# Optimization experiments

Hardware: AMD Instinct MI355X
Metric: run time of the kernel (lower is better)

## Reference

```python
import jax, jax.numpy as jnp
import numpy as np

TOP_K = 6
ROUTED_SCALE = 2.5

def setup_inputs() -> dict:
    key = jax.random.key(0)
    ks = jax.random.split(key, 8)
    T, H, I, E = 1024, 2048, 1024, 16
    Is = 2 * I  # shared expert intermediate = n_shared_experts * moe_intermediate_size
    s = 0.02
    return {
        "hidden_states": jax.random.normal(ks[0], (T, H), jnp.float32),
        "gate_w": jax.random.normal(ks[1], (E, H), jnp.float32) * s,          # ReplicatedLinear [out,in]
        "e_score_correction_bias": jax.random.normal(ks[2], (E,), jnp.float32) * s,
        "w1": jax.random.normal(ks[3], (E, 2 * I, H), jnp.float32) * s,       # merged gate_up per expert
        "w2": jax.random.normal(ks[4], (E, H, I), jnp.float32) * s,           # down proj per expert
        "shared_w1": jax.random.normal(ks[5], (2 * Is, H), jnp.float32) * s,  # shared gate_up
        "shared_w2": jax.random.normal(ks[6], (H, Is), jnp.float32) * s,      # shared down
    }

def _silu_and_mul(gu):
    g, u = jnp.split(gu, 2, axis=-1)
    return jax.nn.silu(g) * u

def _moe_forward(hidden_states, gate_w, e_score_correction_bias, w1, w2, shared_w1, shared_w2):
    T, H = hidden_states.shape
    E = gate_w.shape[0]
    # shared expert path (Dots1MLP)
    shared_out = _silu_and_mul(hidden_states @ shared_w1.T) @ shared_w2.T  # [T,H]
    # gating in fp32 (moe_gating_fp32=True)
    router_logits = hidden_states.astype(jnp.float32) @ gate_w.astype(jnp.float32).T  # [T,E]
    # noaux_tc routing: sigmoid scores + correction bias for selection, raw sigmoid for weights
    scores = jax.nn.sigmoid(router_logits)
    choice = scores + e_score_correction_bias[None, :]
    _, topk_idx = jax.lax.top_k(choice, TOP_K)                              # [T,k]
    topk_w = jnp.take_along_axis(scores, topk_idx, axis=1)                  # [T,k]
    topk_w = topk_w / jnp.sum(topk_w, axis=-1, keepdims=True)
    topk_w = topk_w * ROUTED_SCALE
    # dense combine weights [T,E] (top-k slots per token, rest zero)
    route_w = jnp.zeros((T, E), jnp.float32)
    route_w = route_w.at[jnp.arange(T)[:, None], topk_idx].set(topk_w)
    # expert MLPs (computed for all experts, masked by routing weights)
    gu = jnp.einsum('th,egh->teg', hidden_states, w1)                       # [T,E,2I]
    h = _silu_and_mul(gu)                                                   # [T,E,I]
    routed_out = jnp.einsum('tei,ehi,te->th', h, w2, route_w.astype(hidden_states.dtype))
    return routed_out + shared_out                                          # [T,H]

def reference(hidden_states, gate_w, e_score_correction_bias, w1, w2, shared_w1, shared_w2):
    return _moe_forward(hidden_states, gate_w, e_score_correction_bias, w1, w2, shared_w1, shared_w2)
```

## Files before the change

kernel.cpp:

```cpp
#include <hip/hip_runtime.h>
#include <hip/hip_bf16.h>

#define T_TOK 1024
#define NEXP 16
#define HD 2048
#define TOPK 6

typedef __attribute__((ext_vector_type(8))) short short8;
typedef __attribute__((ext_vector_type(4))) float floatx4;

__device__ __forceinline__ short f2bf(float f) {
    unsigned u = __builtin_bit_cast(unsigned, f);
    u += 0x7FFFu + ((u >> 16) & 1u);
    return (short)(u >> 16);
}

typedef __attribute__((address_space(1))) void gvoid;
typedef __attribute__((address_space(3))) void lvoid;
__device__ __forceinline__ void gload_lds16(const void* g, void* l) {
    __builtin_amdgcn_global_load_lds((gvoid*)g, (lvoid*)l, 16, 0, 0);
}

#define WAITCNT_VM4 0x0F74
#define WAITCNT_VM0 0x0F70

__global__ __launch_bounds__(256) void router_cvt(
    const float* __restrict__ X, const float* __restrict__ GW,
    const float* __restrict__ bias, int* __restrict__ counts,
    int* __restrict__ lists, int* __restrict__ tok_e,
    int* __restrict__ tok_pos, float* __restrict__ tok_w,
    const float* __restrict__ W1, const float* __restrict__ W2,
    const float* __restrict__ SW1, const float* __restrict__ SW2,
    short* __restrict__ Xb, short* __restrict__ W1b, short* __restrict__ W2b,
    short* __restrict__ SW1b, short* __restrict__ SW2b)
{
    if (blockIdx.x < 256) {
        const int wave = threadIdx.x >> 6;
        const int l = threadIdx.x & 63;
        const int t = blockIdx.x * 4 + wave;
        const float* x = X + (size_t)t * HD;
        float acc[NEXP];
#pragma unroll
        for (int e = 0; e < NEXP; ++e) acc[e] = 0.f;
        for (int k = l; k < HD; k += 64) {
            const float xv = x[k];
#pragma unroll
            for (int e = 0; e < NEXP; ++e) acc[e] += xv * GW[e * HD + k];
        }
#pragma unroll
        for (int e = 0; e < NEXP; ++e) {
            float v = acc[e];
#pragma unroll
            for (int m = 32; m >= 1; m >>= 1) v += __shfl_xor(v, m, 64);
            acc[e] = v;
        }
        if (l == 0) {
            float s[NEXP], choice[NEXP];
#pragma unroll
            for (int e = 0; e < NEXP; ++e) {
                s[e] = 1.f / (1.f + __expf(-acc[e]));
                choice[e] = s[e] + bias[e];
            }
            int idx[TOPK]; float wv[TOPK]; float wsum = 0.f;
            bool used[NEXP];
#pragma unroll
            for (int e = 0; e < NEXP; ++e) used[e] = false;
            for (int j = 0; j < TOPK; ++j) {
                float best = -1e30f; int bi = 0;
                for (int e = 0; e < NEXP; ++e)
                    if (!used[e] && choice[e] > best) { best = choice[e]; bi = e; }
                used[bi] = true; idx[j] = bi; wv[j] = s[bi]; wsum += s[bi];
            }
            const float scale = 2.5f / wsum;
            for (int j = 0; j < TOPK; ++j) {
                const int e = idx[j];
                const int pos = atomicAdd(&counts[e], 1);
                lists[e * T_TOK + pos] = t;
                tok_e[t * TOPK + j] = e;
                tok_pos[t * TOPK + j] = pos;
                tok_w[t * TOPK + j] = wv[j] * scale;
            }
        }
        return;
    }
    const int C0 = 262144;
    const int C1 = C0 + 8388608;
    const int C2 = C1 + 4194304;
    const int C3 = C2 + 1048576;
    const int C4 = C3 + 524288;
    const int stride = (gridDim.x - 256) * 256;
#pragma unroll 2
    for (int i = (int)(blockIdx.x - 256) * 256 + (int)threadIdx.x; i < C4;
         i += stride) {
        const float* s; short* d; int l;
        if (i < C0)      { s = X;   d = Xb;   l = i; }
        else if (i < C1) { s = W1;  d = W1b;  l = i - C0; }
        else if (i < C2) { s = W2;  d = W2b;  l = i - C1; }
        else if (i < C3) { s = SW1; d = SW1b; l = i - C2; }
        else             { s = SW2; d = SW2b; l = i - C3; }
        const floatx4 v0 = __builtin_nontemporal_load(((const floatx4*)s) + 2 * l);
        const floatx4 v1 = __builtin_nontemporal_load(((const floatx4*)s) + 2 * l + 1);
        short8 o;
        o[0] = f2bf(v0[0]); o[1] = f2bf(v0[1]); o[2] = f2bf(v0[2]); o[3] = f2bf(v0[3]);
        o[4] = f2bf(v1[0]); o[5] = f2bf(v1[1]); o[6] = f2bf(v1[2]); o[7] = f2bf(v1[3]);
        ((short8*)d)[l] = o;
    }
}

__global__ __launch_bounds__(256) void offsets_descs(
    const int* __restrict__ counts, int* __restrict__ offs,
    int* __restrict__ gu, int* __restrict__ gu_n,
    int* __restrict__ dn, int* __restrict__ dn_n)
{
    __shared__ int base_gu[NEXP], base_dn[NEXP], nys[NEXP];
    if (threadIdx.x == 0) {
        int a = 0, bg = 256, bd = 128;
        for (int e = 0; e < NEXP; ++e) {
            offs[e] = a; a += counts[e];
            const int ny = (counts[e] + 127) >> 7;
            nys[e] = ny; base_gu[e] = bg; base_dn[e] = bd;
            bg += ny * 16; bd += ny * 16;
        }
        *gu_n = bg; *dn_n = bd;
    }
    __syncthreads();
    for (int i = threadIdx.x; i < 256; i += 256)
        gu[i] = (NEXP << 16) | ((i >> 5) << 8) | (i & 31);
    for (int i = threadIdx.x; i < 128; i += 256)
        dn[i] = (NEXP << 16) | ((i >> 4) << 8) | (i & 15);
    for (int e = 0; e < NEXP; ++e) {
        const int nt = nys[e] * 16;
        for (int i = threadIdx.x; i < nt; i += 256) {
            const int v = (e << 16) | ((i >> 4) << 8) | (i & 15);
            gu[base_gu[e] + i] = v;
            dn[base_dn[e] + i] = v;
        }
    }
}

__global__ __launch_bounds__(256) void gateup3(
    const short* __restrict__ Xbf, const short* __restrict__ W1bf,
    const short* __restrict__ SW1bf,
    const int* __restrict__ counts, const int* __restrict__ offs,
    const int* __restrict__ lists, const int* __restrict__ descs,
    const int* __restrict__ ndesc,
    short* __restrict__ h_r, short* __restrict__ h_s)
{
    __shared__ short sA[3][128][32];
    __shared__ short sB[3][128][32];
    if ((int)blockIdx.x >= *ndesc) return;
    const int d = descs[blockIdx.x];
    const int z = d >> 16, yb = (d >> 8) & 255, xb = d & 255;
    const bool shx = (z == NEXP);
    const int cnt = shx ? T_TOK : counts[z];
    const int m0 = yb * 128;
    if (m0 >= cnt) return;
    const int Ih = shx ? 2048 : 1024;
    const int i0 = xb * 64;
    const short* W = shx ? SW1bf : (W1bf + (size_t)z * 2048 * HD);
    short* Hout = shx ? h_s : h_r;
    const int hbase = shx ? 0 : offs[z];

    const int tid = threadIdx.x;
    const int wave = tid >> 6, lane = tid & 63;
    const int srow0 = wave * 32 + (lane >> 2);
    const int srow1 = srow0 + 16;
    const int scol = ((lane & 3) ^ ((lane >> 3) & 3)) * 8;

    int ar0 = m0 + srow0; if (ar0 > cnt - 1) ar0 = cnt - 1;
    int ar1 = m0 + srow1; if (ar1 > cnt - 1) ar1 = cnt - 1;
    const int tok0 = shx ? ar0 : lists[z * T_TOK + ar0];
    const int tok1 = shx ? ar1 : lists[z * T_TOK + ar1];
    const short* ag0 = Xbf + (size_t)tok0 * HD + scol;
    const short* ag1 = Xbf + (size_t)tok1 * HD + scol;
    const int br0 = (srow0 < 64) ? (i0 + srow0) : (Ih + i0 + srow0 - 64);
    const int br1 = (srow1 < 64) ? (i0 + srow1) : (Ih + i0 + srow1 - 64);
    const short* bg0 = W + (size_t)br0 * HD + scol;
    const short* bg1 = W + (size_t)br1 * HD + scol;

    const int wx = wave & 1, wy = wave >> 1;
    const int l15 = lane & 15, l4 = lane >> 4;
    const int fcol = (l4 ^ ((l15 >> 1) & 3)) * 8;

    floatx4 acc[4][4];
#pragma unroll
    for (int a = 0; a < 4; ++a)
#pragma unroll
        for (int b = 0; b < 4; ++b) acc[a][b] = (floatx4){0.f, 0.f, 0.f, 0.f};

    const int nsteps = HD / 32;
#pragma unroll
    for (int pb = 0; pb < 2; ++pb) {
        const int off = pb * 32;
        gload_lds16(ag0 + off, &sA[pb][wave * 32][0]);
        gload_lds16(ag1 + off, &sA[pb][wave * 32 + 16][0]);
        gload_lds16(bg0 + off, &sB[pb][wave * 32][0]);
        gload_lds16(bg1 + off, &sB[pb][wave * 32 + 16][0]);
    }

    int p = 0, q = 2;
    for (int s = 0; s < nsteps; ++s) {
        if (s + 1 < nsteps) __builtin_amdgcn_s_waitcnt(WAITCNT_VM4);
        else                __builtin_amdgcn_s_waitcnt(WAITCNT_VM0);
        __builtin_amdgcn_s_barrier();
        if (s + 2 < nsteps) {
            const int off = (s + 2) * 32;
            gload_lds16(ag0 + off, &sA[q][wave * 32][0]);
            gload_lds16(ag1 + off, &sA[q][wave * 32 + 16][0]);
            gload_lds16(bg0 + off, &sB[q][wave * 32][0]);
            gload_lds16(bg1 + off, &sB[q][wave * 32 + 16][0]);
        }
        short8 af[4], bfr[4];
#pragma unroll
        for (int mc = 0; mc < 4; ++mc)
            af[mc] = *(const short8*)&sA[p][wy * 64 + mc * 16 + l15][fcol];
#pragma unroll
        for (int cb = 0; cb < 4; ++cb) {
            const int br = ((cb < 2) ? 0 : 64) + wx * 32 + (cb & 1) * 16 + l15;
            bfr[cb] = *(const short8*)&sB[p][br][fcol];
        }
#pragma unroll
        for (int mc = 0; mc < 4; ++mc)
#pragma unroll
            for (int cb = 0; cb < 4; ++cb)
                acc[mc][cb] = __builtin_amdgcn_mfma_f32_16x16x32_bf16(
                    af[mc], bfr[cb], acc[mc][cb], 0, 0, 0);
        p = (p == 2) ? 0 : p + 1;
        q = (q == 2) ? 0 : q + 1;
    }

#pragma unroll
    for (int mc = 0; mc < 4; ++mc)
#pragma unroll
        for (int cb = 0; cb < 2; ++cb)
#pragma unroll
            for (int r = 0; r < 4; ++r) {
                const int mrel = wy * 64 + mc * 16 + l4 * 4 + r;
                if (m0 + mrel < cnt) {
                    const float g = acc[mc][cb][r];
                    const float u = acc[mc][cb + 2][r];
                    const float h = g / (1.f + __expf(-g)) * u;
                    const int col = i0 + wx * 32 + cb * 16 + l15;
                    Hout[(size_t)(hbase + m0 + mrel) * Ih + col] = f2bf(h);
                }
            }
}

__global__ __launch_bounds__(256) void down3(
    const short* __restrict__ h_r, const short* __restrict__ h_s,
    const short* __restrict__ W2bf, const short* __restrict__ SW2bf,
    const int* __restrict__ counts, const int* __restrict__ offs,
    const int* __restrict__ descs, const int* __restrict__ ndesc,
    float* __restrict__ h2, float* __restrict__ sh_out)
{
    __shared__ short sA[3][128][32];
    __shared__ short sB[3][128][32];
    if ((int)blockIdx.x >= *ndesc) return;
    const int d = descs[blockIdx.x];
    const int z = d >> 16, yb = (d >> 8) & 255, xb = d & 255;
    const bool shx = (z == NEXP);
    const int cnt = shx ? T_TOK : counts[z];
    const int m0 = yb * 128;
    if (m0 >= cnt) return;
    const int Kih = shx ? 2048 : 1024;
    const int n0 = xb * 128;
    const short* A = shx ? h_s : h_r;
    const short* W = shx ? SW2bf : (W2bf + (size_t)z * HD * 1024);
    float* outb = shx ? sh_out : h2;
    const int hbase = shx ? 0 : offs[z];

    const int tid = threadIdx.x;
    const int wave = tid >> 6, lane = tid & 63;
    const int srow0 = wave * 32 + (lane >> 2);
    const int srow1 = srow0 + 16;
    const int scol = ((lane & 3) ^ ((lane >> 3) & 3)) * 8;

    int ar0 = m0 + srow0; if (ar0 > cnt - 1) ar0 = cnt - 1;
    int ar1 = m0 + srow1; if (ar1 > cnt - 1) ar1 = cnt - 1;
    const short* ag0 = A + (size_t)(hbase + ar0) * Kih + scol;
    const short* ag1 = A + (size_t)(hbase + ar1) * Kih + scol;
    const short* bg0 = W + (size_t)(n0 + srow0) * Kih + scol;
    const short* bg1 = W + (size_t)(n0 + srow1) * Kih + scol;

    const int wx = wave & 1, wy = wave >> 1;
    const int l15 = lane & 15, l4 = lane >> 4;
    const int fcol = (l4 ^ ((l15 >> 1) & 3)) * 8;

    floatx4 acc[4][4];
#pragma unroll
    for (int a = 0; a < 4; ++a)
#pragma unroll
        for (int b = 0; b < 4; ++b) acc[a][b] = (floatx4){0.f, 0.f, 0.f, 0.f};

    const int nsteps = Kih / 32;
#pragma unroll
    for (int pb = 0; pb < 2; ++pb) {
        const int off = pb * 32;
        gload_lds16(ag0 + off, &sA[pb][wave * 32][0]);
        gload_lds16(ag1 + off, &sA[pb][wave * 32 + 16][0]);
        gload_lds16(bg0 + off, &sB[pb][wave * 32][0]);
        gload_lds16(bg1 + off, &sB[pb][wave * 32 + 16][0]);
    }

    int p = 0, q = 2;
    for (int s = 0; s < nsteps; ++s) {
        if (s + 1 < nsteps) __builtin_amdgcn_s_waitcnt(WAITCNT_VM4);
        else                __builtin_amdgcn_s_waitcnt(WAITCNT_VM0);
        __builtin_amdgcn_s_barrier();
        if (s + 2 < nsteps) {
            const int off = (s + 2) * 32;
            gload_lds16(ag0 + off, &sA[q][wave * 32][0]);
            gload_lds16(ag1 + off, &sA[q][wave * 32 + 16][0]);
            gload_lds16(bg0 + off, &sB[q][wave * 32][0]);
            gload_lds16(bg1 + off, &sB[q][wave * 32 + 16][0]);
        }
        short8 af[4], bfr[4];
#pragma unroll
        for (int mc = 0; mc < 4; ++mc)
            af[mc] = *(const short8*)&sA[p][wy * 64 + mc * 16 + l15][fcol];
#pragma unroll
        for (int cb = 0; cb < 4; ++cb)
            bfr[cb] = *(const short8*)&sB[p][wx * 64 + cb * 16 + l15][fcol];
#pragma unroll
        for (int mc = 0; mc < 4; ++mc)
#pragma unroll
            for (int cb = 0; cb < 4; ++cb)
                acc[mc][cb] = __builtin_amdgcn_mfma_f32_16x16x32_bf16(
                    af[mc], bfr[cb], acc[mc][cb], 0, 0, 0);
        p = (p == 2) ? 0 : p + 1;
        q = (q == 2) ? 0 : q + 1;
    }

#pragma unroll
    for (int mc = 0; mc < 4; ++mc)
#pragma unroll
        for (int r = 0; r < 4; ++r) {
            const int mrel = wy * 64 + mc * 16 + l4 * 4 + r;
            if (m0 + mrel >= cnt) continue;
            float* orow = outb + (size_t)(hbase + m0 + mrel) * HD + n0 + wx * 64 + l15;
#pragma unroll
            for (int cb = 0; cb < 4; ++cb)
                orow[cb * 16] = acc[mc][cb][r];
        }
}

__global__ __launch_bounds__(256) void combine_kernel(
    const float* __restrict__ h2, const float* __restrict__ sh_out,
    const int* __restrict__ offs, const int* __restrict__ tok_e,
    const int* __restrict__ tok_pos, const float* __restrict__ tok_w,
    float* __restrict__ out)
{
    const int t = blockIdx.x;
    int rows[TOPK]; float w[TOPK];
#pragma unroll
    for (int j = 0; j < TOPK; ++j) {
        const int e = tok_e[t * TOPK + j];
        rows[j] = offs[e] + tok_pos[t * TOPK + j];
        w[j] = tok_w[t * TOPK + j];
    }
    for (int c = threadIdx.x * 4; c < HD; c += 256 * 4) {
        float4 acc = *(const float4*)(sh_out + (size_t)t * HD + c);
#pragma unroll
        for (int j = 0; j < TOPK; ++j) {
            const float4 v = *(const float4*)(h2 + (size_t)rows[j] * HD + c);
            acc.x += w[j] * v.x; acc.y += w[j] * v.y;
            acc.z += w[j] * v.z; acc.w += w[j] * v.w;
        }
        *(float4*)(out + (size_t)t * HD + c) = acc;
    }
}

extern "C" void kernel_launch(void* const* d_in, const int* in_sizes, int n_in,
                              void* d_out, int out_size, void* d_ws, size_t ws_size,
                              hipStream_t stream) {
    const float* X    = (const float*)d_in[0];
    const float* GW   = (const float*)d_in[1];
    const float* BIAS = (const float*)d_in[2];
    const float* W1   = (const float*)d_in[3];
    const float* W2   = (const float*)d_in[4];
    const float* SW1  = (const float*)d_in[5];
    const float* SW2  = (const float*)d_in[6];
    float* out = (float*)d_out;

    char* ws = (char*)d_ws;
    int*   counts  = (int*)(ws + 0);
    int*   offs    = (int*)(ws + 64);
    int*   lists   = (int*)(ws + 256);
    int*   tok_e   = (int*)(ws + 65792);
    int*   tok_pos = (int*)(ws + 90368);
    float* tok_w   = (float*)(ws + 114944);
    int*   gu_n    = (int*)(ws + 139776);
    int*   dn_n    = (int*)(ws + 139780);
    int*   gu_desc = (int*)(ws + 139840);
    int*   dn_desc = (int*)(ws + 145024);
    short* h_r     = (short*)(ws + 262144);
    short* h_s     = (short*)(ws + 12845056);
    float* h2      = (float*)(ws + 17039360);
    float* sh_out  = (float*)(ws + 67371008);
    short* Xbf     = (short*)(ws + 75759616);
    short* W1bf    = (short*)(ws + 79953920);
    short* W2bf    = (short*)(ws + 214171648);
    short* SW1bf   = (short*)(ws + 281280512);
    short* SW2bf   = (short*)(ws + 298057728);
    const size_t WS_NEEDED = 306446336;
    if (ws_size < WS_NEEDED) return;

    hipMemsetAsync(counts, 0, 64, stream);
    router_cvt<<<4352, 256, 0, stream>>>(X, GW, BIAS, counts, lists,
                                         tok_e, tok_pos, tok_w,
                                         W1, W2, SW1, SW2,
                                         Xbf, W1bf, W2bf, SW1bf, SW2bf);
    offsets_descs<<<1, 256, 0, stream>>>(counts, offs, gu_desc, gu_n,
                                         dn_desc, dn_n);

    gateup3<<<1280, 256, 0, stream>>>(Xbf, W1bf, SW1bf, counts, offs, lists,
                                      gu_desc, gu_n, h_r, h_s);
    down3<<<1152, 256, 0, stream>>>(h_r, h_s, W2bf, SW2bf, counts, offs,
                                    dn_desc, dn_n, h2, sh_out);
    combine_kernel<<<T_TOK, 256, 0, stream>>>(
        h2, sh_out, offs, tok_e, tok_pos, tok_w, out);
}
```

Before: 749.2 us.

## Move W2/SW2 bf16 conversion into gate-up kernel to overlap with GEMM

The fp32-to-bf16 conversion of the down-projection weights (W2, SW2) moves out of the router/convert kernel and into extra blocks appended to the gate-up GEMM launch. That launch grows from 1280 to 3328 blocks, so the memory-bound conversion can run alongside the compute-bound gate-up tiles instead of before them. The remaining X/W1/SW1 conversion also switches from nontemporal loads to plain loads. The risk is that the conversion blocks compete with the GEMM blocks for bandwidth and CU slots, which could delay the GEMM tiles.

```diff
diff --git a/kernel.cpp b/kernel.cpp
--- a/kernel.cpp
+++ b/kernel.cpp
@@ -29,10 +29,8 @@
     const float* __restrict__ bias, int* __restrict__ counts,
     int* __restrict__ lists, int* __restrict__ tok_e,
     int* __restrict__ tok_pos, float* __restrict__ tok_w,
-    const float* __restrict__ W1, const float* __restrict__ W2,
-    const float* __restrict__ SW1, const float* __restrict__ SW2,
-    short* __restrict__ Xb, short* __restrict__ W1b, short* __restrict__ W2b,
-    short* __restrict__ SW1b, short* __restrict__ SW2b)
+    const float* __restrict__ W1, const float* __restrict__ SW1,
+    short* __restrict__ Xb, short* __restrict__ W1b, short* __restrict__ SW1b)
 {
     if (blockIdx.x < 256) {
         const int wave = threadIdx.x >> 6;
@@ -85,21 +83,17 @@
     }
     const int C0 = 262144;
     const int C1 = C0 + 8388608;
-    const int C2 = C1 + 4194304;
-    const int C3 = C2 + 1048576;
-    const int C4 = C3 + 524288;
+    const int C2 = C1 + 1048576;
     const int stride = (gridDim.x - 256) * 256;
 #pragma unroll 2
-    for (int i = (int)(blockIdx.x - 256) * 256 + (int)threadIdx.x; i < C4;
+    for (int i = (int)(blockIdx.x - 256) * 256 + (int)threadIdx.x; i < C2;
          i += stride) {
         const float* s; short* d; int l;
         if (i < C0)      { s = X;   d = Xb;   l = i; }
         else if (i < C1) { s = W1;  d = W1b;  l = i - C0; }
-        else if (i < C2) { s = W2;  d = W2b;  l = i - C1; }
-        else if (i < C3) { s = SW1; d = SW1b; l = i - C2; }
-        else             { s = SW2; d = SW2b; l = i - C3; }
-        const floatx4 v0 = __builtin_nontemporal_load(((const floatx4*)s) + 2 * l);
-        const floatx4 v1 = __builtin_nontemporal_load(((const floatx4*)s) + 2 * l + 1);
+        else             { s = SW1; d = SW1b; l = i - C1; }
+        const floatx4 v0 = ((const floatx4*)s)[2 * l];
+        const floatx4 v1 = ((const floatx4*)s)[2 * l + 1];
         short8 o;
         o[0] = f2bf(v0[0]); o[1] = f2bf(v0[1]); o[2] = f2bf(v0[2]); o[3] = f2bf(v0[3]);
         o[4] = f2bf(v1[0]); o[5] = f2bf(v1[1]); o[6] = f2bf(v1[2]); o[7] = f2bf(v1[3]);
@@ -144,10 +138,31 @@
     const int* __restrict__ counts, const int* __restrict__ offs,
     const int* __restrict__ lists, const int* __restrict__ descs,
     const int* __restrict__ ndesc,
-    short* __restrict__ h_r, short* __restrict__ h_s)
+    short* __restrict__ h_r, short* __restrict__ h_s,
+    const float* __restrict__ W2f, const float* __restrict__ SW2f,
+    short* __restrict__ W2b, short* __restrict__ SW2b)
 {
     __shared__ short sA[3][128][32];
     __shared__ short sB[3][128][32];
+    if (blockIdx.x >= 1280) {
+        const int CW0 = 4194304;
+        const int CW1 = CW0 + 524288;
+        const int stride = ((int)gridDim.x - 1280) * 256;
+#pragma unroll 2
+        for (int i = ((int)blockIdx.x - 1280) * 256 + (int)threadIdx.x;
+             i < CW1; i += stride) {
+            const float* s; short* d; int l;
+            if (i < CW0) { s = W2f;  d = W2b;  l = i; }
+            else         { s = SW2f; d = SW2b; l = i - CW0; }
+            const floatx4 v0 = __builtin_nontemporal_load(((const floatx4*)s) + 2 * l);
+            const floatx4 v1 = __builtin_nontemporal_load(((const floatx4*)s) + 2 * l + 1);
+            short8 o;
+            o[0] = f2bf(v0[0]); o[1] = f2bf(v0[1]); o[2] = f2bf(v0[2]); o[3] = f2bf(v0[3]);
+            o[4] = f2bf(v1[0]); o[5] = f2bf(v1[1]); o[6] = f2bf(v1[2]); o[7] = f2bf(v1[3]);
+            ((short8*)d)[l] = o;
+        }
+        return;
+    }
     if ((int)blockIdx.x >= *ndesc) return;
     const int d = descs[blockIdx.x];
     const int z = d >> 16, yb = (d >> 8) & 255, xb = d & 255;
@@ -408,13 +423,13 @@
     hipMemsetAsync(counts, 0, 64, stream);
     router_cvt<<<4352, 256, 0, stream>>>(X, GW, BIAS, counts, lists,
                                          tok_e, tok_pos, tok_w,
-                                         W1, W2, SW1, SW2,
-                                         Xbf, W1bf, W2bf, SW1bf, SW2bf);
+                                         W1, SW1, Xbf, W1bf, SW1bf);
     offsets_descs<<<1, 256, 0, stream>>>(counts, offs, gu_desc, gu_n,
                                          dn_desc, dn_n);
 
-    gateup3<<<1280, 256, 0, stream>>>(Xbf, W1bf, SW1bf, counts, offs, lists,
-                                      gu_desc, gu_n, h_r, h_s);
+    gateup3<<<3328, 256, 0, stream>>>(Xbf, W1bf, SW1bf, counts, offs, lists,
+                                      gu_desc, gu_n, h_r, h_s,
+                                      W2, SW2, W2bf, SW2bf);
     down3<<<1152, 256, 0, stream>>>(h_r, h_s, W2bf, SW2bf, counts, offs,
                                     dn_desc, dn_n, h2, sh_out);
     combine_kernel<<<T_TOK, 256, 0, stream>>>(
```

New measurement: 747.8 us. Within noise of the previous version (-0.2%).
